# Performance work log

Hardware: AMD Instinct MI355X
Metric: run time of the kernel (lower is better)

The kernel has to match this reference:

```python
import jax, jax.numpy as jnp
import numpy as np

G = 4          # moe_groups
EPG = 4        # experts per group = e_num // moe_groups
E = 16         # e_num
KG = 2         # moe_max_groups
K = 2          # moe_max_k
GTP = 0.9      # moe_group_top_p
TP = 0.9       # moe_top_p
SCALE = 1.0 / float(np.sqrt(G))  # group_scale


def setup_inputs() -> dict:
    key = jax.random.key(0)
    ks = jax.random.split(key, 6)
    B, T, D, H = 2, 1024, 512, 2048  # H = 4*emb_dim per SwiGLU_FFN(emb_dim, 4*emb_dim)
    x = jax.random.normal(ks[0], (B, T, D), jnp.float32)
    Wr = jax.random.normal(ks[1], (D, G), jnp.float32) * 0.02      # group_router weight
    br = jnp.zeros((G,), jnp.float32)                               # group_router bias
    Wgate = jax.random.normal(ks[2], (G, D, EPG), jnp.float32) * 0.02  # per-group gates
    bgate = jnp.zeros((G, EPG), jnp.float32)
    W1 = jax.random.normal(ks[3], (E, D, H), jnp.float32) * 0.02   # SwiGLU gate proj
    W3 = jax.random.normal(ks[4], (E, D, H), jnp.float32) * 0.02   # SwiGLU up proj
    W2 = jax.random.normal(ks[5], (E, H, D), jnp.float32) * 0.02   # SwiGLU down proj
    return {"x": x, "Wr": Wr, "br": br, "Wgate": Wgate, "bgate": bgate,
            "W1": W1, "W3": W3, "W2": W2}


def _routing_weights(xf, Wr, br, Wgate, bgate):
    # Returns combined per-(token, expert) weight (N, E): group_renorm * expert_renorm * SCALE.
    N = xf.shape[0]
    # ---- group-level top-p routing ----
    gp = jax.nn.softmax(xf @ Wr + br, axis=-1)                      # (N, G)
    order = jnp.argsort(-gp, axis=-1)
    sp_k = jnp.take_along_axis(gp, order, axis=-1)[:, :KG]          # top-KG probs, descending
    idx_k = order[:, :KG]
    act = jnp.cumsum(sp_k, axis=-1) <= GTP
    act = act.at[:, 0].set(True)                                    # always keep best group
    mp = sp_k * act
    rn = mp / (jnp.sum(mp, axis=-1, keepdims=True) + 1e-9)
    w_group = jnp.zeros((N, G), xf.dtype).at[jnp.arange(N)[:, None], idx_k].set(rn)
    # ---- expert-level top-p routing within each group ----
    ep = jax.nn.softmax(jnp.einsum('nd,gde->nge', xf, Wgate) + bgate, axis=-1)  # (N, G, EPG)
    eorder = jnp.argsort(-ep, axis=-1)
    esp = jnp.take_along_axis(ep, eorder, axis=-1)[:, :, :K]
    eidx = eorder[:, :, :K]
    eact = jnp.cumsum(esp, axis=-1) <= TP
    eact = eact.at[:, :, 0].set(True)                               # always keep best expert
    emp = esp * eact
    ern = emp / (jnp.sum(emp, axis=-1, keepdims=True) + 1e-9)
    w_exp = jnp.zeros((N, G, EPG), xf.dtype).at[
        jnp.arange(N)[:, None, None], jnp.arange(G)[None, :, None], eidx].set(ern)
    return (w_group[:, :, None] * w_exp * SCALE).reshape(N, E)      # (N, E)


def reference(x, Wr, br, Wgate, bgate, W1, W3, W2):
    B, T, D = x.shape
    xf = x.reshape(-1, D)                                           # (N, D)
    tw = _routing_weights(xf, Wr, br, Wgate, bgate)                 # (N, E)
    out = jnp.zeros_like(xf)
    for e in range(E):  # fixed structural loop over experts
        h = jax.nn.silu(xf @ W1[e]) * (xf @ W3[e])                  # SwiGLU hidden (N, H)
        out = out + tw[:, e:e + 1] * (h @ W2[e])
    return out.reshape(B, T, D)
```

## Files before the change

### kernel.cpp

```cpp
#include <hip/hip_runtime.h>
#include <math.h>

typedef unsigned short u16;
typedef unsigned int   u32;
typedef short s16x8 __attribute__((ext_vector_type(8)));
typedef float f32x4 __attribute__((ext_vector_type(4)));

#define N_TOK 2048
#define DIM   512
#define HID   2048
#define NE    16
#define NG    4
#define EPG   4
#define MAXT  2048

#define BM 64
#define BN 128
#define BK 64

#define WS_CNT    0
#define WS_OFF    128
#define WS_TOKIDX 256
#define WS_TW     (WS_TOKIDX + NE*MAXT*4)
#define WS_XB     (WS_TW + N_TOK*NE*4)
#define WS_HBUF   (WS_XB + (size_t)N_TOK*DIM*2)
#define WS_W1T    (WS_HBUF + (size_t)8192*HID*2)
#define WS_W3T    (WS_W1T + (size_t)NE*HID*DIM*2)
#define WS_W2T    (WS_W3T + (size_t)NE*HID*DIM*2)
#define WS_SLOT   (WS_W2T + (size_t)NE*DIM*HID*2)
#define WS_BUF2   WS_W1T

__device__ __forceinline__ int* ws_i32(void* ws, size_t off) { return (int*)((char*)ws + off); }

__device__ __forceinline__ u16 f2b(float f) {
    union { float f; u32 i; } v; v.f = f;
    u32 b = v.i;
    u32 r = b + 0x7FFFu + ((b >> 16) & 1u);
    return (u16)(r >> 16);
}

__device__ __forceinline__ void gl_lds16(const u16* g, u16* l) {
    __builtin_amdgcn_global_load_lds((const __attribute__((address_space(1))) void*)g,
                                     (__attribute__((address_space(3))) void*)l, 16, 0, 0);
}

__global__ __launch_bounds__(256) void routing_kernel(
    const float* __restrict__ x, const float* __restrict__ Wr, const float* __restrict__ br,
    const float* __restrict__ Wgate, const float* __restrict__ bgate, void* ws)
{
    int tid = threadIdx.x;
    int t = blockIdx.x * 4 + (tid >> 6);
    int lane = tid & 63;

    float xl[8];
    {
        const float4* xr = (const float4*)(x + (size_t)t*DIM + lane*8);
        float4 a = xr[0], b = xr[1];
        xl[0]=a.x; xl[1]=a.y; xl[2]=a.z; xl[3]=a.w;
        xl[4]=b.x; xl[5]=b.y; xl[6]=b.z; xl[7]=b.w;
    }

    {
        union { u16 h[8]; uint4 q; } pk;
        #pragma unroll
        for (int i = 0; i < 8; i++) pk.h[i] = f2b(xl[i]);
        u16* xb = (u16*)((char*)ws + WS_XB);
        *(uint4*)(xb + (size_t)t*DIM + lane*8) = pk.q;
    }

    float gl[NG] = {0.f,0.f,0.f,0.f};
    float el[NE];
    #pragma unroll
    for (int e = 0; e < NE; e++) el[e] = 0.f;

    {
        const float4* Wr4 = (const float4*)Wr;
        #pragma unroll
        for (int c = 0; c < 8; c++) {
            float4 w = Wr4[lane*8 + c];
            gl[0] += xl[c]*w.x; gl[1] += xl[c]*w.y;
            gl[2] += xl[c]*w.z; gl[3] += xl[c]*w.w;
        }
    }
    {
        const float4* Wg4 = (const float4*)Wgate;
        #pragma unroll
        for (int g = 0; g < NG; g++) {
            #pragma unroll
            for (int c = 0; c < 8; c++) {
                float4 w = Wg4[(size_t)g*DIM + lane*8 + c];
                el[g*4+0] += xl[c]*w.x; el[g*4+1] += xl[c]*w.y;
                el[g*4+2] += xl[c]*w.z; el[g*4+3] += xl[c]*w.w;
            }
        }
    }

    #pragma unroll
    for (int g = 0; g < NG; g++)
        #pragma unroll
        for (int s = 32; s; s >>= 1) gl[g] += __shfl_xor(gl[g], s);
    #pragma unroll
    for (int e = 0; e < NE; e++)
        #pragma unroll
        for (int s = 32; s; s >>= 1) el[e] += __shfl_xor(el[e], s);

    if (lane != 0) return;

    float gp[NG];
    float mx = -1e30f;
    #pragma unroll
    for (int g = 0; g < NG; g++) { gl[g] += br[g]; mx = fmaxf(mx, gl[g]); }
    float sum = 0.f;
    #pragma unroll
    for (int g = 0; g < NG; g++) { gp[g] = expf(gl[g] - mx); sum += gp[g]; }
    #pragma unroll
    for (int g = 0; g < NG; g++) gp[g] /= sum;

    int i0 = 0;
    #pragma unroll
    for (int g = 1; g < NG; g++) if (gp[g] > gp[i0]) i0 = g;
    int i1 = -1;
    #pragma unroll
    for (int g = 0; g < NG; g++) { if (g == i0) continue; if (i1 < 0 || gp[g] > gp[i1]) i1 = g; }

    bool act1 = (gp[i0] + gp[i1]) <= 0.9f;
    float mp0 = gp[i0], mp1 = act1 ? gp[i1] : 0.f;
    float inv = 1.f / (mp0 + mp1 + 1e-9f);
    float wg[NG] = {0.f,0.f,0.f,0.f};
    wg[i0] = mp0 * inv;
    wg[i1] = mp1 * inv;

    float tw[NE];
    #pragma unroll
    for (int g = 0; g < NG; g++) {
        float ep[EPG];
        float emx = -1e30f;
        #pragma unroll
        for (int j = 0; j < EPG; j++) {
            float v = el[g*4 + j] + bgate[g*4 + j];
            ep[j] = v; emx = fmaxf(emx, v);
        }
        float es = 0.f;
        #pragma unroll
        for (int j = 0; j < EPG; j++) { ep[j] = expf(ep[j] - emx); es += ep[j]; }
        #pragma unroll
        for (int j = 0; j < EPG; j++) ep[j] /= es;

        int j0 = 0;
        #pragma unroll
        for (int j = 1; j < EPG; j++) if (ep[j] > ep[j0]) j0 = j;
        int j1 = -1;
        #pragma unroll
        for (int j = 0; j < EPG; j++) { if (j == j0) continue; if (j1 < 0 || ep[j] > ep[j1]) j1 = j; }

        bool ea1 = (ep[j0] + ep[j1]) <= 0.9f;
        float e0 = ep[j0], e1 = ea1 ? ep[j1] : 0.f;
        float einv = 1.f / (e0 + e1 + 1e-9f);
        float we[EPG] = {0.f,0.f,0.f,0.f};
        we[j0] = e0 * einv;
        we[j1] = e1 * einv;
        #pragma unroll
        for (int j = 0; j < EPG; j++) tw[g*4 + j] = wg[g] * we[j] * 0.5f;
    }

    float* twT = (float*)((char*)ws + WS_TW);
    #pragma unroll
    for (int e = 0; e < NE; e++) twT[(size_t)e*N_TOK + t] = tw[e];
}

__global__ __launch_bounds__(1024) void expert_scan_kernel(void* ws)
{
    int tid = threadIdx.x;
    int e = tid >> 6, lane = tid & 63;
    const float* twT = (const float*)((char*)ws + WS_TW) + (size_t)e*N_TOK;
    int* tok = ws_i32(ws, WS_TOKIDX) + e*MAXT;
    __shared__ int scnt[NE];
    __shared__ int soff[NE+1];

    float v[32];
    #pragma unroll
    for (int r = 0; r < 32; r++) v[r] = twT[r*64 + lane];

    unsigned long long lanemask = (1ull << lane) - 1ull;
    int base = 0;
    #pragma unroll
    for (int r = 0; r < 32; r++) {
        bool a = v[r] > 0.f;
        unsigned long long m = __ballot(a);
        if (a) tok[base + __popcll(m & lanemask)] = r*64 + lane;
        base += __popcll(m);
    }
    if (lane == 0) scnt[e] = base;
    __syncthreads();
    if (tid == 0) {
        int* cnt = ws_i32(ws, WS_CNT);
        int* off = ws_i32(ws, WS_OFF);
        int s = 0;
        for (int i = 0; i < NE; i++) { cnt[i] = scnt[i]; off[i] = s; soff[i] = s; s += scnt[i]; }
        off[NE] = s; soff[NE] = s;
    }
    __syncthreads();

    int* slot_of = ws_i32(ws, WS_SLOT) + e*N_TOK;
    int base2 = soff[e];
    #pragma unroll
    for (int r = 0; r < 32; r++) {
        bool a = v[r] > 0.f;
        unsigned long long m = __ballot(a);
        int pre = __popcll(m & lanemask);
        slot_of[r*64 + lane] = a ? (base2 + pre) : -1;
        base2 += __popcll(m);
    }
}

__global__ __launch_bounds__(1024) void transpose_all_kernel(
    const float* __restrict__ W1, const float* __restrict__ W3,
    const float* __restrict__ W2, void* ws)
{
    int z = blockIdx.z;
    int mat = z >> 4, e = z & 15;
    int tx = blockIdx.x;
    const float* src; u16* dst; int K, N, k0, n0;
    if (mat == 0)      { src = W1; dst = (u16*)((char*)ws + WS_W1T); K = DIM; N = HID; k0 = (tx>>4)*256; n0 = (tx&15)*128; }
    else if (mat == 1) { src = W3; dst = (u16*)((char*)ws + WS_W3T); K = DIM; N = HID; k0 = (tx>>4)*256; n0 = (tx&15)*128; }
    else               { src = W2; dst = (u16*)((char*)ws + WS_W2T); K = HID; N = DIM; k0 = (tx>>2)*256; n0 = (tx&3)*128; }

    const float* s = src + (size_t)e*K*N;
    u16* d = dst + (size_t)e*N*K;

    __shared__ u16 T[128*256];
    int tid = threadIdx.x;
    int j = tid & 31, i0 = tid >> 5;

    #pragma unroll
    for (int itk = 0; itk < 2; itk++) {
        int kb = 4*i0 + 128*itk;
        const float* base = s + (size_t)(k0 + kb)*N + n0 + 4*j;
        float4 v0 = *(const float4*)(base);
        float4 v1 = *(const float4*)(base + N);
        float4 v2 = *(const float4*)(base + 2*N);
        float4 v3 = *(const float4*)(base + 3*N);
        int c  = (kb >> 2);
        int pc = 4 * (c ^ ((j & 15) << 1));
        union { u16 h[4]; uint2 q; } p;
        p.h[0]=f2b(v0.x); p.h[1]=f2b(v1.x); p.h[2]=f2b(v2.x); p.h[3]=f2b(v3.x);
        *(uint2*)(&T[(4*j+0)*256 + pc]) = p.q;
        p.h[0]=f2b(v0.y); p.h[1]=f2b(v1.y); p.h[2]=f2b(v2.y); p.h[3]=f2b(v3.y);
        *(uint2*)(&T[(4*j+1)*256 + pc]) = p.q;
        p.h[0]=f2b(v0.z); p.h[1]=f2b(v1.z); p.h[2]=f2b(v2.z); p.h[3]=f2b(v3.z);
        *(uint2*)(&T[(4*j+2)*256 + pc]) = p.q;
        p.h[0]=f2b(v0.w); p.h[1]=f2b(v1.w); p.h[2]=f2b(v2.w); p.h[3]=f2b(v3.w);
        *(uint2*)(&T[(4*j+3)*256 + pc]) = p.q;
    }
    __syncthreads();
    #pragma unroll
    for (int it = 0; it < 4; it++) {
        int idx = tid + it*1024;
        int nr = idx >> 5, sg = idx & 31;
        int cp = (2*sg) ^ (((nr >> 2) & 15) << 1);
        *(s16x8*)(d + (size_t)(n0+nr)*K + k0 + sg*8) = *(const s16x8*)(&T[nr*256 + 4*cp]);
    }
}

__global__ __launch_bounds__(256) void gemm1_fast(void* ws)
{
    int e  = blockIdx.z;
    const int* cnt = ws_i32(ws, WS_CNT);
    int ce = cnt[e];
    int m0 = blockIdx.y * BM;
    if (m0 >= ce) return;
    int n0 = blockIdx.x * BN;

    const int* off = ws_i32(ws, WS_OFF);
    const int* tok = ws_i32(ws, WS_TOKIDX) + e*MAXT;
    const u16* xb  = (const u16*)((char*)ws + WS_XB);
    const u16* W1T = (const u16*)((char*)ws + WS_W1T) + (size_t)e*HID*DIM;
    const u16* W3T = (const u16*)((char*)ws + WS_W3T) + (size_t)e*HID*DIM;
    u16* hbuf = (u16*)((char*)ws + WS_HBUF);
    int obase = off[e] + m0;

    __shared__ u16 As[BM*BK];
    __shared__ u16 Bs0[BN*BK];
    __shared__ u16 Bs1[BN*BK];
    __shared__ int rowtok[BM];

    int tid = threadIdx.x;
    if (tid < BM) {
        int m = m0 + tid;
        rowtok[tid] = tok[m < ce ? m : (ce - 1)];
    }
    __syncthreads();

    int wave = tid >> 6, lane = tid & 63;
    int quad = lane >> 4, l16 = lane & 15;
    int swz  = l16 & 7;
    int r8 = lane >> 3, sg = lane & 7;
    int swk = ((sg ^ r8) << 3);

    const u16* arow0 = xb + (size_t)rowtok[wave*16 + r8]*DIM + swk;
    const u16* arow1 = xb + (size_t)rowtok[wave*16 + 8 + r8]*DIM + swk;
    const u16* b1row[4]; const u16* b3row[4];
    #pragma unroll
    for (int i = 0; i < 4; i++) {
        size_t nr = (size_t)(n0 + wave*32 + i*8 + r8)*DIM + swk;
        b1row[i] = W1T + nr;
        b3row[i] = W3T + nr;
    }

    f32x4 acc1[4][2], acc3[4][2];
    #pragma unroll
    for (int mt = 0; mt < 4; mt++)
        #pragma unroll
        for (int nt = 0; nt < 2; nt++) {
            acc1[mt][nt] = (f32x4){0.f,0.f,0.f,0.f};
            acc3[mt][nt] = (f32x4){0.f,0.f,0.f,0.f};
        }

    for (int k0 = 0; k0 < DIM; k0 += BK) {
        gl_lds16(arow0 + k0, &As[(wave*16)*BK]);
        gl_lds16(arow1 + k0, &As[(wave*16 + 8)*BK]);
        #pragma unroll
        for (int i = 0; i < 4; i++) {
            gl_lds16(b1row[i] + k0, &Bs0[(wave*32 + i*8)*BK]);
            gl_lds16(b3row[i] + k0, &Bs1[(wave*32 + i*8)*BK]);
        }
        __syncthreads();

        #pragma unroll
        for (int kk = 0; kk < BK; kk += 32) {
            int jj = (kk >> 3) + quad;
            int so = ((jj ^ swz) << 3);
            s16x8 af[4];
            #pragma unroll
            for (int mt = 0; mt < 4; mt++)
                af[mt] = *(const s16x8*)(&As[(mt*16 + l16)*BK + so]);
            #pragma unroll
            for (int nt = 0; nt < 2; nt++) {
                int n = wave*32 + nt*16 + l16;
                s16x8 b1 = *(const s16x8*)(&Bs0[n*BK + so]);
                s16x8 b3 = *(const s16x8*)(&Bs1[n*BK + so]);
                #pragma unroll
                for (int mt = 0; mt < 4; mt++) {
                    acc1[mt][nt] = __builtin_amdgcn_mfma_f32_16x16x32_bf16(af[mt], b1, acc1[mt][nt], 0, 0, 0);
                    acc3[mt][nt] = __builtin_amdgcn_mfma_f32_16x16x32_bf16(af[mt], b3, acc3[mt][nt], 0, 0, 0);
                }
            }
        }
        __syncthreads();
    }

    #pragma unroll
    for (int mt = 0; mt < 4; mt++) {
        #pragma unroll
        for (int r = 0; r < 4; r++) {
            int row = mt*16 + quad*4 + r;
            if (m0 + row < ce) {
                #pragma unroll
                for (int nt = 0; nt < 2; nt++) {
                    float a = acc1[mt][nt][r];
                    float b = acc3[mt][nt][r];
                    float h = (a / (1.f + expf(-a))) * b;
                    int col = wave*32 + nt*16 + l16;
                    hbuf[(size_t)(obase + row)*HID + n0 + col] = f2b(h);
                }
            }
        }
    }
}

__global__ __launch_bounds__(256) void gemm2_fast(void* ws)
{
    int e  = blockIdx.z;
    const int* cnt = ws_i32(ws, WS_CNT);
    int ce = cnt[e];
    int m0 = blockIdx.y * BM;
    if (m0 >= ce) return;
    int n0 = blockIdx.x * BN;

    const int* off = ws_i32(ws, WS_OFF);
    const int* tok = ws_i32(ws, WS_TOKIDX) + e*MAXT;
    const float* twT = (const float*)((char*)ws + WS_TW);
    const u16* hbuf = (const u16*)((char*)ws + WS_HBUF);
    const u16* W2T = (const u16*)((char*)ws + WS_W2T) + (size_t)e*DIM*HID;
    float* buf2 = (float*)((char*)ws + WS_BUF2);
    int abase = off[e] + m0;
    int total = off[NE];

    __shared__ u16 As[BM*BK];
    __shared__ u16 Bs[BN*BK];

    int tid = threadIdx.x;
    int wave = tid >> 6, lane = tid & 63;
    int quad = lane >> 4, l16 = lane & 15;
    int swz  = l16 & 7;
    int r8 = lane >> 3, sg = lane & 7;
    int swk = ((sg ^ r8) << 3);

    int ar0 = abase + wave*16 + r8;      if (ar0 > total - 1) ar0 = total - 1;
    int ar1 = abase + wave*16 + 8 + r8;  if (ar1 > total - 1) ar1 = total - 1;
    const u16* arow0 = hbuf + (size_t)ar0*HID + swk;
    const u16* arow1 = hbuf + (size_t)ar1*HID + swk;
    const u16* brow[4];
    #pragma unroll
    for (int i = 0; i < 4; i++)
        brow[i] = W2T + (size_t)(n0 + wave*32 + i*8 + r8)*HID + swk;

    f32x4 acc[4][2];
    #pragma unroll
    for (int mt = 0; mt < 4; mt++)
        #pragma unroll
        for (int nt = 0; nt < 2; nt++) acc[mt][nt] = (f32x4){0.f,0.f,0.f,0.f};

    for (int k0 = 0; k0 < HID; k0 += BK) {
        gl_lds16(arow0 + k0, &As[(wave*16)*BK]);
        gl_lds16(arow1 + k0, &As[(wave*16 + 8)*BK]);
        #pragma unroll
        for (int i = 0; i < 4; i++)
            gl_lds16(brow[i] + k0, &Bs[(wave*32 + i*8)*BK]);
        __syncthreads();

        #pragma unroll
        for (int kk = 0; kk < BK; kk += 32) {
            int jj = (kk >> 3) + quad;
            int so = ((jj ^ swz) << 3);
            s16x8 af[4];
            #pragma unroll
            for (int mt = 0; mt < 4; mt++)
                af[mt] = *(const s16x8*)(&As[(mt*16 + l16)*BK + so]);
            #pragma unroll
            for (int nt = 0; nt < 2; nt++) {
                int n = wave*32 + nt*16 + l16;
                s16x8 bfr = *(const s16x8*)(&Bs[n*BK + so]);
                #pragma unroll
                for (int mt = 0; mt < 4; mt++)
                    acc[mt][nt] = __builtin_amdgcn_mfma_f32_16x16x32_bf16(af[mt], bfr, acc[mt][nt], 0, 0, 0);
            }
        }
        __syncthreads();
    }

    #pragma unroll
    for (int mt = 0; mt < 4; mt++) {
        #pragma unroll
        for (int r = 0; r < 4; r++) {
            int row = mt*16 + quad*4 + r;
            if (m0 + row < ce) {
                int t = tok[m0 + row];
                float s = twT[(size_t)e*N_TOK + t];
                #pragma unroll
                for (int nt = 0; nt < 2; nt++) {
                    int col = wave*32 + nt*16 + l16;
                    buf2[(size_t)(abase + row)*DIM + n0 + col] = acc[mt][nt][r] * s;
                }
            }
        }
    }
}

__global__ __launch_bounds__(128) void gather_kernel(void* ws, float* __restrict__ out)
{
    int t = blockIdx.x;
    int tid = threadIdx.x;
    const int* slot_of = ws_i32(ws, WS_SLOT);
    const float* buf2 = (const float*)((char*)ws + WS_BUF2);

    int d = tid * 4;
    float4 acc = {0.f, 0.f, 0.f, 0.f};
    #pragma unroll
    for (int e = 0; e < NE; e++) {
        int s = slot_of[e*N_TOK + t];
        if (s >= 0) {
            float4 v = *(const float4*)(buf2 + (size_t)s*DIM + d);
            acc.x += v.x; acc.y += v.y; acc.z += v.z; acc.w += v.w;
        }
    }
    *(float4*)(out + (size_t)t*DIM + d) = acc;
}

extern "C" void kernel_launch(void* const* d_in, const int* in_sizes, int n_in,
                              void* d_out, int out_size, void* d_ws, size_t ws_size,
                              hipStream_t stream)
{
    const float* x     = (const float*)d_in[0];
    const float* Wr    = (const float*)d_in[1];
    const float* br    = (const float*)d_in[2];
    const float* Wgate = (const float*)d_in[3];
    const float* bgate = (const float*)d_in[4];
    const float* W1    = (const float*)d_in[5];
    const float* W3    = (const float*)d_in[6];
    const float* W2    = (const float*)d_in[7];
    float* out = (float*)d_out;

    transpose_all_kernel<<<dim3(32, 1, 48), 1024, 0, stream>>>(W1, W3, W2, d_ws);
    routing_kernel<<<N_TOK/4, 256, 0, stream>>>(x, Wr, br, Wgate, bgate, d_ws);
    expert_scan_kernel<<<1, 1024, 0, stream>>>(d_ws);
    gemm1_fast<<<dim3(HID/BN, N_TOK/BM, NE), 256, 0, stream>>>(d_ws);
    gemm2_fast<<<dim3(DIM/BN, N_TOK/BM, NE), 256, 0, stream>>>(d_ws);
    gather_kernel<<<N_TOK, 128, 0, stream>>>(d_ws, out);
}
```

Baseline: 357.7 us.

## Pipeline weight transpose with multi-tile blocks and double-buffered LDS

The weight transpose/bf16 conversion kernel now has each block process six 128x128 tiles in sequence, instead of one 256x128 tile per block. The tiles alternate between two LDS buffers, and the global loads for the next tile are issued before the current tile is written out. This is meant to hide global read latency behind the LDS transpose and stores, and to cut the number of block launches. In exchange it uses fewer blocks (512), so less parallelism is available to hide latency, and a raw s_barrier with a manual waitcnt replaces __syncthreads.

```diff
diff --git a/kernel.cpp b/kernel.cpp
--- a/kernel.cpp
+++ b/kernel.cpp
@@ -217,48 +217,62 @@
     const float* __restrict__ W1, const float* __restrict__ W3,
     const float* __restrict__ W2, void* ws)
 {
-    int z = blockIdx.z;
-    int mat = z >> 4, e = z & 15;
-    int tx = blockIdx.x;
-    const float* src; u16* dst; int K, N, k0, n0;
-    if (mat == 0)      { src = W1; dst = (u16*)((char*)ws + WS_W1T); K = DIM; N = HID; k0 = (tx>>4)*256; n0 = (tx&15)*128; }
-    else if (mat == 1) { src = W3; dst = (u16*)((char*)ws + WS_W3T); K = DIM; N = HID; k0 = (tx>>4)*256; n0 = (tx&15)*128; }
-    else               { src = W2; dst = (u16*)((char*)ws + WS_W2T); K = HID; N = DIM; k0 = (tx>>2)*256; n0 = (tx&3)*128; }
-
-    const float* s = src + (size_t)e*K*N;
-    u16* d = dst + (size_t)e*N*K;
-
-    __shared__ u16 T[128*256];
+    __shared__ u16 T[2][128*128];
     int tid = threadIdx.x;
     int j = tid & 31, i0 = tid >> 5;
-
-    #pragma unroll
-    for (int itk = 0; itk < 2; itk++) {
-        int kb = 4*i0 + 128*itk;
-        const float* base = s + (size_t)(k0 + kb)*N + n0 + 4*j;
-        float4 v0 = *(const float4*)(base);
-        float4 v1 = *(const float4*)(base + N);
-        float4 v2 = *(const float4*)(base + 2*N);
-        float4 v3 = *(const float4*)(base + 3*N);
-        int c  = (kb >> 2);
-        int pc = 4 * (c ^ ((j & 15) << 1));
+    int tg0 = blockIdx.x * 6;
+
+    const float* src; u16* dst; int K, N, k0, n0;
+    float4 v0, v1, v2, v3;
+
+    auto setup = [&](int tg) {
+        int z = tg >> 6, w = tg & 63;
+        int mat = z >> 4, e = z & 15;
+        if (mat == 0)      { src = W1; dst = (u16*)((char*)ws + WS_W1T); }
+        else if (mat == 1) { src = W3; dst = (u16*)((char*)ws + WS_W3T); }
+        else               { src = W2; dst = (u16*)((char*)ws + WS_W2T); }
+        if (mat < 2) { K = DIM; N = HID; k0 = (w & 3)  << 7; n0 = (w >> 2) << 7; }
+        else         { K = HID; N = DIM; k0 = (w & 15) << 7; n0 = (w >> 4) << 7; }
+        src += (size_t)e*K*N + (size_t)(k0 + 4*i0)*N + n0 + 4*j;
+        dst += (size_t)e*N*K;
+    };
+    auto issue_loads = [&]() {
+        v0 = *(const float4*)(src);
+        v1 = *(const float4*)(src + N);
+        v2 = *(const float4*)(src + 2*N);
+        v3 = *(const float4*)(src + 3*N);
+    };
+
+    setup(tg0);
+    issue_loads();
+
+    for (int it = 0; it < 6; ++it) {
+        u16* dstc = dst; int Kc = K, k0c = k0, n0c = n0;
+        u16* Tb = &T[it & 1][0];
+
+        int pc = 4 * (i0 ^ ((j & 15) << 1));
         union { u16 h[4]; uint2 q; } p;
         p.h[0]=f2b(v0.x); p.h[1]=f2b(v1.x); p.h[2]=f2b(v2.x); p.h[3]=f2b(v3.x);
-        *(uint2*)(&T[(4*j+0)*256 + pc]) = p.q;
+        *(uint2*)(&Tb[(4*j+0)*128 + pc]) = p.q;
         p.h[0]=f2b(v0.y); p.h[1]=f2b(v1.y); p.h[2]=f2b(v2.y); p.h[3]=f2b(v3.y);
-        *(uint2*)(&T[(4*j+1)*256 + pc]) = p.q;
+        *(uint2*)(&Tb[(4*j+1)*128 + pc]) = p.q;
         p.h[0]=f2b(v0.z); p.h[1]=f2b(v1.z); p.h[2]=f2b(v2.z); p.h[3]=f2b(v3.z);
-        *(uint2*)(&T[(4*j+2)*256 + pc]) = p.q;
+        *(uint2*)(&Tb[(4*j+2)*128 + pc]) = p.q;
         p.h[0]=f2b(v0.w); p.h[1]=f2b(v1.w); p.h[2]=f2b(v2.w); p.h[3]=f2b(v3.w);
-        *(uint2*)(&T[(4*j+3)*256 + pc]) = p.q;
-    }
-    __syncthreads();
-    #pragma unroll
-    for (int it = 0; it < 4; it++) {
-        int idx = tid + it*1024;
-        int nr = idx >> 5, sg = idx & 31;
-        int cp = (2*sg) ^ (((nr >> 2) & 15) << 1);
-        *(s16x8*)(d + (size_t)(n0+nr)*K + k0 + sg*8) = *(const s16x8*)(&T[nr*256 + 4*cp]);
+        *(uint2*)(&Tb[(4*j+3)*128 + pc]) = p.q;
+
+        if (it + 1 < 6) { setup(tg0 + it + 1); issue_loads(); }
+
+        asm volatile("s_waitcnt lgkmcnt(0)" ::: "memory");
+        __builtin_amdgcn_s_barrier();
+
+        #pragma unroll
+        for (int ph = 0; ph < 2; ++ph) {
+            int idx = tid + ph*1024;
+            int nr = idx >> 4, sg = idx & 15;
+            int cp = (2*sg) ^ (((nr >> 2) & 15) << 1);
+            *(s16x8*)(dstc + (size_t)(n0c + nr)*Kc + k0c + sg*8) = *(const s16x8*)(&Tb[nr*128 + 4*cp]);
+        }
     }
 }
 
@@ -491,7 +505,7 @@
     const float* W2    = (const float*)d_in[7];
     float* out = (float*)d_out;
 
-    transpose_all_kernel<<<dim3(32, 1, 48), 1024, 0, stream>>>(W1, W3, W2, d_ws);
+    transpose_all_kernel<<<dim3(512), 1024, 0, stream>>>(W1, W3, W2, d_ws);
     routing_kernel<<<N_TOK/4, 256, 0, stream>>>(x, Wr, br, Wgate, bgate, d_ws);
     expert_scan_kernel<<<1, 1024, 0, stream>>>(d_ws);
     gemm1_fast<<<dim3(HID/BN, N_TOK/BM, NE), 256, 0, stream>>>(d_ws);
```

Result: no change. 358.4 us (+0.2%).
